# Performance work log

Measured on AMD Instinct MI355X. Metric: run time of the kernel, lower is better.

Reference implementation:

```python
import jax, jax.numpy as jnp
import numpy as np

N, D, H, L, E, P = 50000, 128, 128, 3, 640000, 100000


def setup_inputs() -> dict:
    key = jax.random.key(0)
    ks = jax.random.split(key, 10)
    x = jax.random.normal(ks[0], (N, D), dtype=jnp.float32)
    ei = jax.random.randint(ks[1], (2, E), 0, N, dtype=jnp.int64)
    pos = jax.random.randint(ks[2], (2, P), 0, N, dtype=jnp.int64)
    neg = jax.random.randint(ks[3], (2, P), 0, N, dtype=jnp.int64)
    # GCN weights: layer0 is [D,H], rest [H,H]; D==H so stack as [L,H,H]
    gcn_w = jax.random.normal(ks[4], (L, H, H), dtype=jnp.float32) / np.sqrt(H)
    gcn_b = jnp.zeros((L, H), dtype=jnp.float32)
    pred_w = jax.random.normal(ks[5], (H * L, 1), dtype=jnp.float32) / np.sqrt(H * L)
    pred_b = jnp.zeros((1,), dtype=jnp.float32)
    return {"x": x, "ei": ei, "pos": pos, "neg": neg,
            "gcn_w": gcn_w, "gcn_b": gcn_b, "pred_w": pred_w, "pred_b": pred_b}


def reference(x, ei, pos, neg, gcn_w, gcn_b, pred_w, pred_b):
    n = x.shape[0]
    loops = jnp.arange(n, dtype=ei.dtype)
    src = jnp.concatenate([ei[0], loops])  # self-loops (GCNConv default)
    dst = jnp.concatenate([ei[1], loops])
    deg = jax.ops.segment_sum(jnp.ones_like(dst, dtype=x.dtype), dst, num_segments=n)
    dinv = jax.lax.rsqrt(deg)  # deg >= 1 thanks to self-loops
    coef = (dinv[src] * dinv[dst])[:, None]  # [E+N, 1] symmetric norm

    embs = []
    h = x
    for i in range(gcn_w.shape[0]):
        hw = h @ gcn_w[i]                                   # [N, H]
        agg = jax.ops.segment_sum(hw[src] * coef, dst, num_segments=n)
        h = jax.nn.relu(agg + gcn_b[i])
        embs.append(h)
    z = jnp.concatenate(embs, axis=1)                        # [N, H*L]

    def logits(e):
        return (z[e[0]] * z[e[1]]) @ pred_w + pred_b         # [P, 1]

    pos_logit = logits(pos)
    neg_logit = logits(neg)
    # BCEWithLogitsLoss with targets [1...1, 0...0], mean reduction
    total = pos_logit.shape[0] + neg_logit.shape[0]
    loss = (jnp.sum(-jax.nn.log_sigmoid(pos_logit)) +
            jnp.sum(-jax.nn.log_sigmoid(-neg_logit))) / total
    return loss
```

## Files before the change

kernel.cpp:

```cpp
#include <hip/hip_runtime.h>
#include <hip/hip_bf16.h>

#define DD 128

typedef __attribute__((ext_vector_type(8))) short short8;
typedef __attribute__((ext_vector_type(4))) float f32x4;
typedef __attribute__((ext_vector_type(2))) float f32x2;

static __device__ __forceinline__ int gtid() {
    return blockIdx.x * blockDim.x + threadIdx.x;
}

static __device__ __forceinline__ ushort f2bfu(float f) {
    __hip_bfloat16 h = __float2bfloat16(f);
    return *reinterpret_cast<ushort*>(&h);
}

static __device__ __forceinline__ unsigned int fp8e(float f) {
    unsigned int s = (__float_as_uint(f) >> 31) << 7;
    float a = fabsf(f);
    if (a < 0.015625f) return s | (unsigned int)rintf(a * 512.0f);
    unsigned int u = __float_as_uint(a);
    u += 0x0007FFFFu + ((u >> 20) & 1u);
    unsigned int e8 = (u >> 23) - 120u;
    unsigned int m = (u >> 20) & 7u;
    if (e8 > 15u || (e8 == 15u && m == 7u)) return s | 0x7Eu;
    return s | (e8 << 3) | m;
}

static __device__ __forceinline__ float fp8d(unsigned int b) {
    unsigned int t = b & 0x7Fu;
    float v = (t >= 8u) ? __uint_as_float((t << 20) + 0x3C000000u)
                        : (float)t * 0.001953125f;
    return (b & 0x80u) ? -v : v;
}

static __device__ __forceinline__ unsigned int pk8x2(float a, float b) {
#if __has_builtin(__builtin_amdgcn_cvt_pk_fp8_f32)
    return (unsigned int)__builtin_amdgcn_cvt_pk_fp8_f32(a, b, 0, false);
#else
    return fp8e(a) | (fp8e(b) << 8);
#endif
}

static __device__ __forceinline__ unsigned int pk8x4(float a, float b, float c, float d) {
#if __has_builtin(__builtin_amdgcn_cvt_pk_fp8_f32)
    int v = __builtin_amdgcn_cvt_pk_fp8_f32(a, b, 0, false);
    v = __builtin_amdgcn_cvt_pk_fp8_f32(c, d, v, true);
    return (unsigned int)v;
#else
    return fp8e(a) | (fp8e(b) << 8) | (fp8e(c) << 16) | (fp8e(d) << 24);
#endif
}

static __device__ __forceinline__ void fp8x4_dec(unsigned int u, float* f) {
#if __has_builtin(__builtin_amdgcn_cvt_pk_f32_fp8)
    f32x2 lo = __builtin_amdgcn_cvt_pk_f32_fp8((int)u, false);
    f32x2 hi = __builtin_amdgcn_cvt_pk_f32_fp8((int)u, true);
    f[0] = lo[0]; f[1] = lo[1]; f[2] = hi[0]; f[3] = hi[1];
#else
    f[0] = fp8d(u & 0xFFu);
    f[1] = fp8d((u >> 8) & 0xFFu);
    f[2] = fp8d((u >> 16) & 0xFFu);
    f[3] = fp8d((u >> 24) & 0xFFu);
#endif
}


__global__ void count_kernel(int* __restrict__ counts, const int* __restrict__ dst, int e) {
    int i = gtid();
    if (i < e) atomicAdd(&counts[dst[i]], 1);
}

__global__ __launch_bounds__(256) void scan_blocks(const int* __restrict__ counts,
                                                   int* __restrict__ rowptr,
                                                   int* __restrict__ partial,
                                                   float* __restrict__ dinv, int n) {
    __shared__ int s[256];
    int i = blockIdx.x * 256 + threadIdx.x;
    int v = (i < n) ? counts[i] : 0;
    if (i < n) dinv[i] = rsqrtf(1.0f + (float)v);
    s[threadIdx.x] = v;
    __syncthreads();
    for (int off = 1; off < 256; off <<= 1) {
        int t = (threadIdx.x >= off) ? s[threadIdx.x - off] : 0;
        __syncthreads();
        s[threadIdx.x] += t;
        __syncthreads();
    }
    if (i < n) rowptr[i] = s[threadIdx.x] - v;
    if (threadIdx.x == 255) partial[blockIdx.x] = s[255];
}

__global__ __launch_bounds__(256) void scan_partials(int* __restrict__ partial,
                                                     int* __restrict__ partial2, int nb) {
    __shared__ int s[256];
    int v = (threadIdx.x < nb) ? partial[threadIdx.x] : 0;
    s[threadIdx.x] = v;
    __syncthreads();
    for (int off = 1; off < 256; off <<= 1) {
        int t = (threadIdx.x >= off) ? s[threadIdx.x - off] : 0;
        __syncthreads();
        s[threadIdx.x] += t;
        __syncthreads();
    }
    partial2[threadIdx.x] = s[threadIdx.x] - v;
}

__global__ __launch_bounds__(256) void add_offsets(int* __restrict__ rowptr,
                                                   int* __restrict__ cursor,
                                                   const int* __restrict__ partial2,
                                                   int n, int e) {
    int i = blockIdx.x * 256 + threadIdx.x;
    if (i < n) {
        int r = rowptr[i] + partial2[blockIdx.x];
        rowptr[i] = r;
        cursor[i] = r;
        if (i == n - 1) rowptr[n] = e;
    }
}

__global__ __launch_bounds__(256) void fill_kernel(
    const int* __restrict__ ei, int* __restrict__ cursor,
    ushort* __restrict__ csr_src, int e, int n, int blocksPerPart) {
    int part = blockIdx.x & 7;
    int blk = blockIdx.x >> 3;
    int lo = (int)(((long)n * part) >> 3);
    int hi = (int)(((long)n * (part + 1)) >> 3);
    int stride = blocksPerPart * 256;
    for (int i = blk * 256 + threadIdx.x; i < e; i += stride) {
        int d = ei[e + i];
        if (d < lo || d >= hi) continue;
        int s = ei[i];
        int pos = atomicAdd(&cursor[d], 1);
        csr_src[pos] = (ushort)s;
    }
}

__global__ void cvt_kernel(const float* __restrict__ x, unsigned char* __restrict__ xq, size_t m8) {
    size_t i = (size_t)blockIdx.x * blockDim.x + threadIdx.x;
    if (i >= m8) return;
    const float4* xp = reinterpret_cast<const float4*>(x + i * 8);
    float4 a = xp[0], b = xp[1];
    uint2 q;
    q.x = pk8x4(a.x, a.y, a.z, a.w);
    q.y = pk8x4(b.x, b.y, b.z, b.w);
    *reinterpret_cast<uint2*>(xq + i * 8) = q;
}

__global__ __launch_bounds__(256) void wpack_kernel(const float* __restrict__ gcn_w,
                                                    ushort* __restrict__ wfrag) {
    int tid = blockIdx.x * 256 + threadIdx.x;
    if (tid >= 3 * 4 * 8 * 64) return;
    int lane = tid & 63;
    int c = (tid >> 6) & 7;
    int s = (tid >> 9) & 3;
    int l = tid >> 11;
    const float* W = gcn_w + (size_t)l * 128 * 128;
    int col = c * 16 + (lane & 15);
    int k0 = s * 32 + (lane >> 4) * 8;
    ushort u[8];
#pragma unroll
    for (int j = 0; j < 8; ++j) {
        u[j] = f2bfu(W[(size_t)(k0 + j) * 128 + col]);
    }
    *reinterpret_cast<uint4*>(wfrag + (size_t)tid * 8) = *reinterpret_cast<const uint4*>(u);
}

__global__ __launch_bounds__(256) void aggregate_fp8_kernel(
    const unsigned char* __restrict__ srcq, int srcStride, const int* __restrict__ rowptr,
    const ushort* __restrict__ csr_src, const float* __restrict__ dinv,
    ushort* __restrict__ aggh, int n) {
    int gid = gtid();
    int row = gid >> 6;
    if (row >= n) return;
    int lane = threadIdx.x & 63;
    int g = lane >> 3;
    int c = lane & 7;
    int j0 = rowptr[row], j1 = rowptr[row + 1];
    float dr = dinv[row];
    float acc[16];
#pragma unroll
    for (int k = 0; k < 16; ++k) acc[k] = 0.f;
    for (int j = j0 + g; j < j1; j += 8) {
        int s = (int)csr_src[j];
        float cf = dinv[s] * dr;
        uint4 v = *reinterpret_cast<const uint4*>(srcq + (size_t)s * srcStride + c * 16);
        float f[16];
        fp8x4_dec(v.x, f);
        fp8x4_dec(v.y, f + 4);
        fp8x4_dec(v.z, f + 8);
        fp8x4_dec(v.w, f + 12);
#pragma unroll
        for (int k = 0; k < 16; ++k) acc[k] = fmaf(cf, f[k], acc[k]);
    }
#pragma unroll
    for (int k = 0; k < 16; ++k) {
        acc[k] += __shfl_xor(acc[k], 8);
        acc[k] += __shfl_xor(acc[k], 16);
        acc[k] += __shfl_xor(acc[k], 32);
    }
    float d2 = dr * dr;
    uint4 sv = *reinterpret_cast<const uint4*>(srcq + (size_t)row * srcStride + c * 16);
    float sf[16];
    fp8x4_dec(sv.x, sf);
    fp8x4_dec(sv.y, sf + 4);
    fp8x4_dec(sv.z, sf + 8);
    fp8x4_dec(sv.w, sf + 12);
#pragma unroll
    for (int k = 0; k < 16; ++k) acc[k] = fmaf(d2, sf[k], acc[k]);
    if (g == 0) {
        unsigned int pk[8];
#pragma unroll
        for (int q = 0; q < 8; ++q) {
            pk[q] = (unsigned int)f2bfu(acc[2 * q]) | ((unsigned int)f2bfu(acc[2 * q + 1]) << 16);
        }
        ushort* ap = aggh + (size_t)row * 128 + c * 16;
        *reinterpret_cast<uint4*>(ap) = *reinterpret_cast<const uint4*>(pk);
        *reinterpret_cast<uint4*>(ap + 8) = *reinterpret_cast<const uint4*>(pk + 4);
    }
}

__global__ __launch_bounds__(256) void gemm_mfma_kernel(
    const ushort* __restrict__ aggh, const ushort* __restrict__ wfrag,
    const float* __restrict__ bias, const float* __restrict__ pwsl,
    unsigned char* __restrict__ zq_sl, unsigned char* __restrict__ zqw_sl, int ntiles) {
    int lane = threadIdx.x & 63;
    int wv = threadIdx.x >> 6;
    short8 b0[4], b1[4];
    int c0 = wv * 2;
#pragma unroll
    for (int s = 0; s < 4; ++s) {
        b0[s] = *reinterpret_cast<const short8*>(wfrag + ((size_t)(s * 8 + c0) * 64 + lane) * 8);
        b1[s] = *reinterpret_cast<const short8*>(wfrag + ((size_t)(s * 8 + c0 + 1) * 64 + lane) * 8);
    }
    int rlo = lane & 15;
    int kg = lane >> 4;
    int col0 = wv * 32 + rlo;
    int col1 = col0 + 16;
    float bias0 = bias[col0], bias1 = bias[col1];
    float pw0 = pwsl[col0] * 8.0f, pw1 = pwsl[col1] * 8.0f;
    for (int rt = blockIdx.x; rt < ntiles; rt += gridDim.x) {
        const ushort* ap = aggh + (size_t)(rt * 16 + rlo) * 128 + kg * 8;
        short8 a0 = *reinterpret_cast<const short8*>(ap);
        short8 a1 = *reinterpret_cast<const short8*>(ap + 32);
        short8 a2 = *reinterpret_cast<const short8*>(ap + 64);
        short8 a3 = *reinterpret_cast<const short8*>(ap + 96);
        f32x4 acc0 = {0.f, 0.f, 0.f, 0.f};
        f32x4 acc1 = {0.f, 0.f, 0.f, 0.f};
        acc0 = __builtin_amdgcn_mfma_f32_16x16x32_bf16(a0, b0[0], acc0, 0, 0, 0);
        acc1 = __builtin_amdgcn_mfma_f32_16x16x32_bf16(a0, b1[0], acc1, 0, 0, 0);
        acc0 = __builtin_amdgcn_mfma_f32_16x16x32_bf16(a1, b0[1], acc0, 0, 0, 0);
        acc1 = __builtin_amdgcn_mfma_f32_16x16x32_bf16(a1, b1[1], acc1, 0, 0, 0);
        acc0 = __builtin_amdgcn_mfma_f32_16x16x32_bf16(a2, b0[2], acc0, 0, 0, 0);
        acc1 = __builtin_amdgcn_mfma_f32_16x16x32_bf16(a2, b1[2], acc1, 0, 0, 0);
        acc0 = __builtin_amdgcn_mfma_f32_16x16x32_bf16(a3, b0[3], acc0, 0, 0, 0);
        acc1 = __builtin_amdgcn_mfma_f32_16x16x32_bf16(a3, b1[3], acc1, 0, 0, 0);
        int row0 = rt * 16 + kg * 4;
#pragma unroll
        for (int r = 0; r < 4; ++r) {
            float v0 = fmaxf(acc0[r] + bias0, 0.f);
            float v1 = fmaxf(acc1[r] + bias1, 0.f);
            unsigned int q = pk8x2(v0, v1);
            unsigned char* zr = zq_sl + (size_t)(row0 + r) * 384 + col0;
            zr[0] = (unsigned char)(q & 0xFFu);
            zr[16] = (unsigned char)((q >> 8) & 0xFFu);
            unsigned int w = pk8x2(v0 * pw0, v1 * pw1);
            unsigned char* wr = zqw_sl + (size_t)(row0 + r) * 384 + col0;
            wr[0] = (unsigned char)(w & 0xFFu);
            wr[16] = (unsigned char)((w >> 8) & 0xFFu);
        }
    }
}

__global__ __launch_bounds__(256) void loss_mfma_kernel(
    const unsigned char* __restrict__ zq, const unsigned char* __restrict__ zqw,
    const int* __restrict__ pos, const int* __restrict__ neg,
    const float* __restrict__ pb, float* __restrict__ partialOut,
    int p, float inv_total) {
    __shared__ float red[4];
    int lane = threadIdx.x & 63;
    int wv = threadIdx.x >> 6;
    int pairBase = (blockIdx.x * 4 + wv) * 16;
    float term = 0.f;
    if (pairBase < 2 * p) {
        int m = lane & 15;
        int kg = lane >> 4;
        int pi = pairBase + m;
        int pic = (pi < 2 * p) ? pi : (2 * p - 1);
        bool isneg = (pic >= p);
        const int* pr = isneg ? neg : pos;
        int idx = isneg ? (pic - p) : pic;
        int a = pr[idx];
        int b = pr[p + idx];
        const long* pa = reinterpret_cast<const long*>(zq + (size_t)a * 384) + kg;
        const long* pbw = reinterpret_cast<const long*>(zqw + (size_t)b * 384) + kg;
        long av[12], bv[12];
#pragma unroll
        for (int s = 0; s < 12; ++s) av[s] = pa[s * 4];
#pragma unroll
        for (int s = 0; s < 12; ++s) bv[s] = pbw[s * 4];
        f32x4 acc = {0.f, 0.f, 0.f, 0.f};
#pragma unroll
        for (int s = 0; s < 12; ++s) {
            acc = __builtin_amdgcn_mfma_f32_16x16x32_fp8_fp8(av[s], bv[s], acc, 0, 0, 0);
        }
        bool isdiag = (lane >> 4) == ((lane & 15) >> 2);
        int r2 = lane & 3;
        float v = (r2 == 0) ? acc[0] : (r2 == 1) ? acc[1] : (r2 == 2) ? acc[2] : acc[3];
        if (isdiag && pi < 2 * p) {
            float logit = v * 0.125f + pb[0];
            float t = isneg ? logit : -logit;
            term = (fmaxf(t, 0.f) + log1pf(expf(-fabsf(t)))) * inv_total;
        }
    }
#pragma unroll
    for (int off = 1; off < 64; off <<= 1) term += __shfl_xor(term, off);
    if (lane == 0) red[wv] = term;
    __syncthreads();
    if (threadIdx.x == 0) partialOut[blockIdx.x] = red[0] + red[1] + red[2] + red[3];
}

__global__ __launch_bounds__(256) void loss_reduce_kernel(
    const float* __restrict__ partial, float* __restrict__ out, int m) {
    __shared__ float s[256];
    float a = 0.f;
    for (int i = threadIdx.x; i < m; i += 256) a += partial[i];
    s[threadIdx.x] = a;
    __syncthreads();
    for (int off = 128; off > 0; off >>= 1) {
        if (threadIdx.x < off) s[threadIdx.x] += s[threadIdx.x + off];
        __syncthreads();
    }
    if (threadIdx.x == 0) out[0] = s[0];
}

extern "C" void kernel_launch(void* const* d_in, const int* in_sizes, int n_in,
                              void* d_out, int out_size, void* d_ws, size_t ws_size,
                              hipStream_t stream) {
    const float* x      = (const float*)d_in[0];
    const int*   ei     = (const int*)d_in[1];
    const int*   pos    = (const int*)d_in[2];
    const int*   neg    = (const int*)d_in[3];
    const float* gcn_w  = (const float*)d_in[4];
    const float* gcn_b  = (const float*)d_in[5];
    const float* pred_w = (const float*)d_in[6];
    const float* pred_b = (const float*)d_in[7];
    float* out = (float*)d_out;

    const int n = in_sizes[0] / DD;
    const int e = in_sizes[1] / 2;
    const int p = in_sizes[2] / 2;
    const int nb = (n + 255) / 256;

    char* ws = (char*)d_ws;
    size_t off = 0;
    auto alloc = [&](size_t bytes) {
        void* ptr = ws + off;
        off += (bytes + 255) & ~(size_t)255;
        return ptr;
    };
    float* dinv      = (float*)alloc((size_t)n * 4);
    int*   counts    = (int*)alloc((size_t)n * 4);
    int*   rowptr    = (int*)alloc((size_t)(n + 1) * 4);
    int*   cursor    = (int*)alloc((size_t)n * 4);
    int*   partial   = (int*)alloc(256 * 4);
    int*   partial2  = (int*)alloc(256 * 4);
    float* lossPart  = (float*)alloc((size_t)4096 * 4);
    ushort* csr_src  = (ushort*)alloc((size_t)e * 2);
    ushort* wfrag    = (ushort*)alloc((size_t)3 * 2048 * 8 * 2);
    unsigned char* xq = (unsigned char*)alloc((size_t)n * 128);
    ushort* aggh = (ushort*)alloc((size_t)n * 128 * 2);
    unsigned char* zq  = (unsigned char*)alloc((size_t)n * 384);
    unsigned char* zqw = (unsigned char*)alloc((size_t)n * 384);
    (void)ws_size;

    hipMemsetAsync(counts, 0, (size_t)n * 4, stream);

    count_kernel<<<(e + 255) / 256, 256, 0, stream>>>(counts, ei + e, e);
    scan_blocks<<<nb, 256, 0, stream>>>(counts, rowptr, partial, dinv, n);
    scan_partials<<<1, 256, 0, stream>>>(partial, partial2, nb);
    add_offsets<<<nb, 256, 0, stream>>>(rowptr, cursor, partial2, n, e);
    int blocksPerPart = (e + 255) / 256 / 2;
    fill_kernel<<<blocksPerPart * 8, 256, 0, stream>>>(ei, cursor, csr_src, e, n, blocksPerPart);

    size_t m8 = (size_t)n * 128 / 8;
    cvt_kernel<<<(int)((m8 + 255) / 256), 256, 0, stream>>>(x, xq, m8);
    wpack_kernel<<<24, 256, 0, stream>>>(gcn_w, wfrag);

    const int ntiles = n / 16;
    const int aggBlocks = (n * 64 + 255) / 256;
    for (int l = 0; l < 3; ++l) {
        const unsigned char* srcq = (l == 0) ? xq : (zq + (size_t)(l - 1) * 128);
        int srcStride = (l == 0) ? 128 : 384;
        aggregate_fp8_kernel<<<aggBlocks, 256, 0, stream>>>(
            srcq, srcStride, rowptr, csr_src, dinv, aggh, n);
        gemm_mfma_kernel<<<ntiles, 256, 0, stream>>>(
            aggh, wfrag + (size_t)l * 2048 * 8,
            gcn_b + (size_t)l * 128, pred_w + (size_t)l * 128,
            zq + (size_t)l * 128, zqw + (size_t)l * 128, ntiles);
    }

    float inv_total = 1.0f / (2.0f * (float)p);
    int lossBlocks = (2 * p + 63) / 64;
    loss_mfma_kernel<<<lossBlocks, 256, 0, stream>>>(
        zq, zqw, pos, neg, pred_b, lossPart, p, inv_total);
    loss_reduce_kernel<<<1, 256, 0, stream>>>(lossPart, out, lossBlocks);
}
```

Baseline: 255.6 us.

## Fuse sparse aggregation and MFMA GEMM into one per-layer kernel via LDS

Merges the per-layer aggregate and GEMM kernels into a single kernel. Each block aggregates 16 rows (four per wave) into a swizzled LDS tile, synchronises, then runs the bf16 MFMA transform and writes the fp8 outputs. This drops the global bf16 intermediate buffer, its write and read traffic, and one launch per layer. In exchange each wave now handles four rows one after another, and the GEMM waits at a barrier on the slowest row in the block, which may reduce latency hiding in the gather phase.

Result: slower. 264.0 us (+3.3%).

```diff
diff --git a/kernel.cpp b/kernel.cpp
--- a/kernel.cpp
+++ b/kernel.cpp
@@ -167,109 +167,114 @@
     *reinterpret_cast<uint4*>(wfrag + (size_t)tid * 8) = *reinterpret_cast<const uint4*>(u);
 }
 
-__global__ __launch_bounds__(256) void aggregate_fp8_kernel(
-    const unsigned char* __restrict__ srcq, int srcStride, const int* __restrict__ rowptr,
-    const ushort* __restrict__ csr_src, const float* __restrict__ dinv,
-    ushort* __restrict__ aggh, int n) {
-    int gid = gtid();
-    int row = gid >> 6;
-    if (row >= n) return;
+__global__ __launch_bounds__(256) void layer_fused_kernel(
+    const unsigned char* __restrict__ srcq, int srcStride,
+    const int* __restrict__ rowptr, const ushort* __restrict__ csr_src,
+    const float* __restrict__ dinv, const ushort* __restrict__ wfrag,
+    const float* __restrict__ bias, const float* __restrict__ pwsl,
+    unsigned char* __restrict__ zq_sl, unsigned char* __restrict__ zqw_sl, int n) {
+    __shared__ unsigned char ah[16 * 256];
     int lane = threadIdx.x & 63;
-    int g = lane >> 3;
-    int c = lane & 7;
-    int j0 = rowptr[row], j1 = rowptr[row + 1];
-    float dr = dinv[row];
-    float acc[16];
-#pragma unroll
-    for (int k = 0; k < 16; ++k) acc[k] = 0.f;
-    for (int j = j0 + g; j < j1; j += 8) {
-        int s = (int)csr_src[j];
-        float cf = dinv[s] * dr;
-        uint4 v = *reinterpret_cast<const uint4*>(srcq + (size_t)s * srcStride + c * 16);
-        float f[16];
-        fp8x4_dec(v.x, f);
-        fp8x4_dec(v.y, f + 4);
-        fp8x4_dec(v.z, f + 8);
-        fp8x4_dec(v.w, f + 12);
-#pragma unroll
-        for (int k = 0; k < 16; ++k) acc[k] = fmaf(cf, f[k], acc[k]);
-    }
-#pragma unroll
-    for (int k = 0; k < 16; ++k) {
-        acc[k] += __shfl_xor(acc[k], 8);
-        acc[k] += __shfl_xor(acc[k], 16);
-        acc[k] += __shfl_xor(acc[k], 32);
-    }
-    float d2 = dr * dr;
-    uint4 sv = *reinterpret_cast<const uint4*>(srcq + (size_t)row * srcStride + c * 16);
-    float sf[16];
-    fp8x4_dec(sv.x, sf);
-    fp8x4_dec(sv.y, sf + 4);
-    fp8x4_dec(sv.z, sf + 8);
-    fp8x4_dec(sv.w, sf + 12);
-#pragma unroll
-    for (int k = 0; k < 16; ++k) acc[k] = fmaf(d2, sf[k], acc[k]);
-    if (g == 0) {
-        unsigned int pk[8];
-#pragma unroll
-        for (int q = 0; q < 8; ++q) {
-            pk[q] = (unsigned int)f2bfu(acc[2 * q]) | ((unsigned int)f2bfu(acc[2 * q + 1]) << 16);
-        }
-        ushort* ap = aggh + (size_t)row * 128 + c * 16;
-        *reinterpret_cast<uint4*>(ap) = *reinterpret_cast<const uint4*>(pk);
-        *reinterpret_cast<uint4*>(ap + 8) = *reinterpret_cast<const uint4*>(pk + 4);
-    }
-}
-
-__global__ __launch_bounds__(256) void gemm_mfma_kernel(
-    const ushort* __restrict__ aggh, const ushort* __restrict__ wfrag,
-    const float* __restrict__ bias, const float* __restrict__ pwsl,
-    unsigned char* __restrict__ zq_sl, unsigned char* __restrict__ zqw_sl, int ntiles) {
-    int lane = threadIdx.x & 63;
-    int wv = threadIdx.x >> 6;
+    int wid = threadIdx.x >> 6;
+    int row0 = blockIdx.x * 16;
+
     short8 b0[4], b1[4];
-    int c0 = wv * 2;
+    int c0 = wid * 2;
 #pragma unroll
     for (int s = 0; s < 4; ++s) {
         b0[s] = *reinterpret_cast<const short8*>(wfrag + ((size_t)(s * 8 + c0) * 64 + lane) * 8);
         b1[s] = *reinterpret_cast<const short8*>(wfrag + ((size_t)(s * 8 + c0 + 1) * 64 + lane) * 8);
     }
+
+    int g = lane >> 3;
+    int c = lane & 7;
+#pragma unroll
+    for (int t = 0; t < 4; ++t) {
+        int lr = wid * 4 + t;
+        int row = row0 + lr;
+        int j0 = rowptr[row], j1 = rowptr[row + 1];
+        float dr = dinv[row];
+        float acc[16];
+#pragma unroll
+        for (int k = 0; k < 16; ++k) acc[k] = 0.f;
+        for (int j = j0 + g; j < j1; j += 8) {
+            int s = (int)csr_src[j];
+            float cf = dinv[s] * dr;
+            uint4 v = *reinterpret_cast<const uint4*>(srcq + (size_t)s * srcStride + c * 16);
+            float f[16];
+            fp8x4_dec(v.x, f);
+            fp8x4_dec(v.y, f + 4);
+            fp8x4_dec(v.z, f + 8);
+            fp8x4_dec(v.w, f + 12);
+#pragma unroll
+            for (int k = 0; k < 16; ++k) acc[k] = fmaf(cf, f[k], acc[k]);
+        }
+#pragma unroll
+        for (int k = 0; k < 16; ++k) {
+            acc[k] += __shfl_xor(acc[k], 8);
+            acc[k] += __shfl_xor(acc[k], 16);
+            acc[k] += __shfl_xor(acc[k], 32);
+        }
+        float d2 = dr * dr;
+        uint4 sv = *reinterpret_cast<const uint4*>(srcq + (size_t)row * srcStride + c * 16);
+        float sf[16];
+        fp8x4_dec(sv.x, sf);
+        fp8x4_dec(sv.y, sf + 4);
+        fp8x4_dec(sv.z, sf + 8);
+        fp8x4_dec(sv.w, sf + 12);
+#pragma unroll
+        for (int k = 0; k < 16; ++k) acc[k] = fmaf(d2, sf[k], acc[k]);
+        if (g == 0) {
+            unsigned int pk[8];
+#pragma unroll
+            for (int q = 0; q < 8; ++q) {
+                pk[q] = (unsigned int)f2bfu(acc[2 * q]) | ((unsigned int)f2bfu(acc[2 * q + 1]) << 16);
+            }
+            int swz = (lr & 7) << 4;
+            int bo = c * 32;
+            *reinterpret_cast<uint4*>(ah + lr * 256 + (bo ^ swz)) =
+                *reinterpret_cast<const uint4*>(pk);
+            *reinterpret_cast<uint4*>(ah + lr * 256 + ((bo + 16) ^ swz)) =
+                *reinterpret_cast<const uint4*>(pk + 4);
+        }
+    }
+    __syncthreads();
+
     int rlo = lane & 15;
     int kg = lane >> 4;
-    int col0 = wv * 32 + rlo;
-    int col1 = col0 + 16;
-    float bias0 = bias[col0], bias1 = bias[col1];
-    float pw0 = pwsl[col0] * 8.0f, pw1 = pwsl[col1] * 8.0f;
-    for (int rt = blockIdx.x; rt < ntiles; rt += gridDim.x) {
-        const ushort* ap = aggh + (size_t)(rt * 16 + rlo) * 128 + kg * 8;
-        short8 a0 = *reinterpret_cast<const short8*>(ap);
-        short8 a1 = *reinterpret_cast<const short8*>(ap + 32);
-        short8 a2 = *reinterpret_cast<const short8*>(ap + 64);
-        short8 a3 = *reinterpret_cast<const short8*>(ap + 96);
-        f32x4 acc0 = {0.f, 0.f, 0.f, 0.f};
-        f32x4 acc1 = {0.f, 0.f, 0.f, 0.f};
-        acc0 = __builtin_amdgcn_mfma_f32_16x16x32_bf16(a0, b0[0], acc0, 0, 0, 0);
-        acc1 = __builtin_amdgcn_mfma_f32_16x16x32_bf16(a0, b1[0], acc1, 0, 0, 0);
-        acc0 = __builtin_amdgcn_mfma_f32_16x16x32_bf16(a1, b0[1], acc0, 0, 0, 0);
-        acc1 = __builtin_amdgcn_mfma_f32_16x16x32_bf16(a1, b1[1], acc1, 0, 0, 0);
-        acc0 = __builtin_amdgcn_mfma_f32_16x16x32_bf16(a2, b0[2], acc0, 0, 0, 0);
-        acc1 = __builtin_amdgcn_mfma_f32_16x16x32_bf16(a2, b1[2], acc1, 0, 0, 0);
-        acc0 = __builtin_amdgcn_mfma_f32_16x16x32_bf16(a3, b0[3], acc0, 0, 0, 0);
-        acc1 = __builtin_amdgcn_mfma_f32_16x16x32_bf16(a3, b1[3], acc1, 0, 0, 0);
-        int row0 = rt * 16 + kg * 4;
-#pragma unroll
-        for (int r = 0; r < 4; ++r) {
-            float v0 = fmaxf(acc0[r] + bias0, 0.f);
-            float v1 = fmaxf(acc1[r] + bias1, 0.f);
-            unsigned int q = pk8x2(v0, v1);
-            unsigned char* zr = zq_sl + (size_t)(row0 + r) * 384 + col0;
-            zr[0] = (unsigned char)(q & 0xFFu);
-            zr[16] = (unsigned char)((q >> 8) & 0xFFu);
-            unsigned int w = pk8x2(v0 * pw0, v1 * pw1);
-            unsigned char* wr = zqw_sl + (size_t)(row0 + r) * 384 + col0;
-            wr[0] = (unsigned char)(w & 0xFFu);
-            wr[16] = (unsigned char)((w >> 8) & 0xFFu);
-        }
+    int swzr = (rlo & 7) << 4;
+    const unsigned char* arow = ah + rlo * 256;
+    short8 a0 = *reinterpret_cast<const short8*>(arow + ((kg * 16) ^ swzr));
+    short8 a1 = *reinterpret_cast<const short8*>(arow + ((kg * 16 + 64) ^ swzr));
+    short8 a2 = *reinterpret_cast<const short8*>(arow + ((kg * 16 + 128) ^ swzr));
+    short8 a3 = *reinterpret_cast<const short8*>(arow + ((kg * 16 + 192) ^ swzr));
+    f32x4 acc0 = {0.f, 0.f, 0.f, 0.f};
+    f32x4 acc1 = {0.f, 0.f, 0.f, 0.f};
+    acc0 = __builtin_amdgcn_mfma_f32_16x16x32_bf16(a0, b0[0], acc0, 0, 0, 0);
+    acc1 = __builtin_amdgcn_mfma_f32_16x16x32_bf16(a0, b1[0], acc1, 0, 0, 0);
+    acc0 = __builtin_amdgcn_mfma_f32_16x16x32_bf16(a1, b0[1], acc0, 0, 0, 0);
+    acc1 = __builtin_amdgcn_mfma_f32_16x16x32_bf16(a1, b1[1], acc1, 0, 0, 0);
+    acc0 = __builtin_amdgcn_mfma_f32_16x16x32_bf16(a2, b0[2], acc0, 0, 0, 0);
+    acc1 = __builtin_amdgcn_mfma_f32_16x16x32_bf16(a2, b1[2], acc1, 0, 0, 0);
+    acc0 = __builtin_amdgcn_mfma_f32_16x16x32_bf16(a3, b0[3], acc0, 0, 0, 0);
+    acc1 = __builtin_amdgcn_mfma_f32_16x16x32_bf16(a3, b1[3], acc1, 0, 0, 0);
+
+    int col0 = wid * 32 + rlo;
+    float bias0 = bias[col0], bias1 = bias[col0 + 16];
+    float pw0 = pwsl[col0] * 8.0f, pw1 = pwsl[col0 + 16] * 8.0f;
+    int rowBase = row0 + kg * 4;
+#pragma unroll
+    for (int r = 0; r < 4; ++r) {
+        float v0 = fmaxf(acc0[r] + bias0, 0.f);
+        float v1 = fmaxf(acc1[r] + bias1, 0.f);
+        unsigned int q = pk8x2(v0, v1);
+        unsigned char* zr = zq_sl + (size_t)(rowBase + r) * 384 + col0;
+        zr[0] = (unsigned char)(q & 0xFFu);
+        zr[16] = (unsigned char)((q >> 8) & 0xFFu);
+        unsigned int w = pk8x2(v0 * pw0, v1 * pw1);
+        unsigned char* wr = zqw_sl + (size_t)(rowBase + r) * 384 + col0;
+        wr[0] = (unsigned char)(w & 0xFFu);
+        wr[16] = (unsigned char)((w >> 8) & 0xFFu);
     }
 }
 
@@ -370,7 +375,6 @@
     ushort* csr_src  = (ushort*)alloc((size_t)e * 2);
     ushort* wfrag    = (ushort*)alloc((size_t)3 * 2048 * 8 * 2);
     unsigned char* xq = (unsigned char*)alloc((size_t)n * 128);
-    ushort* aggh = (ushort*)alloc((size_t)n * 128 * 2);
     unsigned char* zq  = (unsigned char*)alloc((size_t)n * 384);
     unsigned char* zqw = (unsigned char*)alloc((size_t)n * 384);
     (void)ws_size;
@@ -388,17 +392,15 @@
     cvt_kernel<<<(int)((m8 + 255) / 256), 256, 0, stream>>>(x, xq, m8);
     wpack_kernel<<<24, 256, 0, stream>>>(gcn_w, wfrag);
 
-    const int ntiles = n / 16;
-    const int aggBlocks = (n * 64 + 255) / 256;
+    const int layerBlocks = n / 16;
     for (int l = 0; l < 3; ++l) {
         const unsigned char* srcq = (l == 0) ? xq : (zq + (size_t)(l - 1) * 128);
         int srcStride = (l == 0) ? 128 : 384;
-        aggregate_fp8_kernel<<<aggBlocks, 256, 0, stream>>>(
-            srcq, srcStride, rowptr, csr_src, dinv, aggh, n);
-        gemm_mfma_kernel<<<ntiles, 256, 0, stream>>>(
-            aggh, wfrag + (size_t)l * 2048 * 8,
+        layer_fused_kernel<<<layerBlocks, 256, 0, stream>>>(
+            srcq, srcStride, rowptr, csr_src, dinv,
+            wfrag + (size_t)l * 2048 * 8,
             gcn_b + (size_t)l * 128, pred_w + (size_t)l * 128,
-            zq + (size_t)l * 128, zqw + (size_t)l * 128, ntiles);
+            zq + (size_t)l * 128, zqw + (size_t)l * 128, n);
     }
 
     float inv_total = 1.0f / (2.0f * (float)p);
```
